# Kernel optimization log

Measured on AMD Instinct MI355X. Metric: run time of the kernel, lower is better.

The kernel has to match this reference:

```python
import jax, jax.numpy as jnp
import numpy as np

N, E = 30000, 480000
HID, NB, D = 256, 128, 2
SW = D * D * NB        # struct-encoder width = bundle_dim^2 * num_bundles = 512
NL, NSAGE = 2, 5       # outer BDL layers, SAGE layers inside struct encoder
OUT = 5
EPS = 1e-5


def _gelu(x):
    return jax.nn.gelu(x, approximate=False)  # torch nn.GELU default (exact)


def _mean_agg(x, src, dst):
    # mean over incoming edges: agg[v] = mean_{u->v} x[u]
    s = jax.ops.segment_sum(x[src], dst, num_segments=N)
    deg = jax.ops.segment_sum(jnp.ones((E,), x.dtype), dst, num_segments=N)
    return s / jnp.maximum(deg, 1.0)[:, None]


def _layernorm(x, g, b):
    m = jnp.mean(x, -1, keepdims=True)
    v = jnp.mean((x - m) ** 2, -1, keepdims=True)
    return (x - m) * jax.lax.rsqrt(v + EPS) * g + b


def _householder(X):
    # torch.nn.utils.parametrizations Orthogonal, orthogonal_map='householder':
    # Q = H_0 H_1 ... H_{d-1}, H_i = I - tau_i v_i v_i^T, v_i = strict-lower col i with unit diag
    d = X.shape[-1]
    A = jnp.tril(X, k=-1)
    tau = 2.0 / (1.0 + jnp.sum(A * A, axis=-2))  # [M, d]
    eye = jnp.eye(d, dtype=X.dtype)
    Q = jnp.broadcast_to(eye, X.shape)
    for i in range(d):
        v = A[:, :, i] + eye[i]
        Qv = jnp.einsum('mij,mj->mi', Q, v)
        Q = Q - tau[:, i, None, None] * Qv[:, :, None] * v[:, None, :]
    return Q


def _struct_encoder(h, src, dst, se_in_w, se_in_b, sage_w1, sage_b1, sage_w2, sage_b2, se_out_w, se_out_b):
    # Model('SAGE', 5, ...) with normalization='None'; dropout inactive in eval
    z = _gelu(h @ se_in_w + se_in_b)
    for i in range(NSAGE):
        m = _mean_agg(z, src, dst)
        zc = jnp.concatenate([z, m], axis=-1)  # SAGE: cat(self, mean(neigh))
        z = z + (_gelu(zc @ sage_w1[i] + sage_b1[i]) @ sage_w2[i] + sage_b2[i])
    return z @ se_out_w + se_out_b


def _forward(x, w_in, b_in, se_in_w, se_in_b, sage_w1, sage_b1, sage_w2, sage_b2,
             se_out_w, se_out_b, enc_w1, enc_b1, enc_w2, enc_b2, ln_g, ln_b,
             bdl_w1, bdl_b1, bdl_w2, bdl_b2, out_ln_g, out_ln_b, w_out, b_out, edge_index):
    src, dst = edge_index[0], edge_index[1]
    h = _gelu(x @ w_in + b_in)
    for k in range(NL):
        enc = _struct_encoder(h, src, dst, se_in_w, se_in_b, sage_w1, sage_b1,
                              sage_w2, sage_b2, se_out_w, se_out_b)
        nr = _gelu(enc @ enc_w1[k] + enc_b1[k]) @ enc_w2[k] + enc_b2[k]  # [N, SW]
        O = _householder(nr.reshape(N * NB, D, D)).reshape(N, NB, D, D)
        # BDL residual module: transport features through per-node bundle frames
        hn = _layernorm(h, ln_g[k], ln_b[k])
        hb = hn.reshape(N, NB, D)
        y = jnp.einsum('nbij,nbj->nbi', O, hb)                       # rotate into frame
        agg = _mean_agg(y.reshape(N, NB * D), src, dst).reshape(N, NB, D)
        msg = jnp.einsum('nbji,nbj->nbi', O, agg).reshape(N, NB * D)  # O^T transports back
        hc = jnp.concatenate([hn, msg], axis=-1)
        h = h + (_gelu(hc @ bdl_w1[k] + bdl_b1[k]) @ bdl_w2[k] + bdl_b2[k])
    h = _layernorm(h, out_ln_g, out_ln_b)
    return h @ w_out + b_out  # [N, OUT]; .squeeze(1) is a no-op for OUT>1


def _w(key, fan_in, shape):
    return jax.random.normal(key, shape, dtype=jnp.float32) / np.sqrt(fan_in)


def setup_inputs() -> dict:
    key = jax.random.key(0)
    ks = iter(jax.random.split(key, 40))
    f32 = jnp.float32
    return {
        'x': jax.random.normal(next(ks), (N, HID), dtype=f32),
        'edge_index': jax.random.randint(next(ks), (2, E), 0, N, dtype=jnp.int32),
        'w_in': _w(next(ks), HID, (HID, HID)), 'b_in': jnp.zeros((HID,), f32),
        'se_in_w': _w(next(ks), HID, (HID, SW)), 'se_in_b': jnp.zeros((SW,), f32),
        'sage_w1': _w(next(ks), 2 * SW, (NSAGE, 2 * SW, SW)), 'sage_b1': jnp.zeros((NSAGE, SW), f32),
        'sage_w2': _w(next(ks), SW, (NSAGE, SW, SW)), 'sage_b2': jnp.zeros((NSAGE, SW), f32),
        'se_out_w': _w(next(ks), SW, (SW, SW)), 'se_out_b': jnp.zeros((SW,), f32),
        'enc_w1': _w(next(ks), SW, (NL, SW, SW)), 'enc_b1': jnp.zeros((NL, SW), f32),
        'enc_w2': _w(next(ks), SW, (NL, SW, SW)), 'enc_b2': jnp.zeros((NL, SW), f32),
        'ln_g': jnp.ones((NL, HID), f32), 'ln_b': jnp.zeros((NL, HID), f32),
        'bdl_w1': _w(next(ks), 2 * HID, (NL, 2 * HID, HID)), 'bdl_b1': jnp.zeros((NL, HID), f32),
        'bdl_w2': _w(next(ks), HID, (NL, HID, HID)), 'bdl_b2': jnp.zeros((NL, HID), f32),
        'out_ln_g': jnp.ones((HID,), f32), 'out_ln_b': jnp.zeros((HID,), f32),
        'w_out': _w(next(ks), HID, (HID, OUT)), 'b_out': jnp.zeros((OUT,), f32),
    }


def reference(x, edge_index, w_in, b_in, se_in_w, se_in_b, sage_w1, sage_b1, sage_w2, sage_b2,
              se_out_w, se_out_b, enc_w1, enc_b1, enc_w2, enc_b2, ln_g, ln_b,
              bdl_w1, bdl_b1, bdl_w2, bdl_b2, out_ln_g, out_ln_b, w_out, b_out):
    return _forward(x, w_in, b_in, se_in_w, se_in_b, sage_w1, sage_b1, sage_w2, sage_b2,
                    se_out_w, se_out_b, enc_w1, enc_b1, enc_w2, enc_b2, ln_g, ln_b,
                    bdl_w1, bdl_b1, bdl_w2, bdl_b2, out_ln_g, out_ln_b, w_out, b_out, edge_index)
```

## Files before the change

kernel.cpp:

```cpp
#include <hip/hip_runtime.h>
#include <hip/hip_bf16.h>
#include <cstdint>
#include <cstddef>


typedef __attribute__((ext_vector_type(8))) short short8;
typedef __attribute__((ext_vector_type(4))) float f32x4;

__device__ __forceinline__ float gelu_exact(float x) {
  return 0.5f * x * (1.0f + erff(x * 0.7071067811865475f));
}
__device__ __forceinline__ unsigned short f2bf(float f) {
  __hip_bfloat16 b = __float2bfloat16(f);
  return *reinterpret_cast<unsigned short*>(&b);
}
__device__ __forceinline__ float bf2f(unsigned short u) {
  return __uint_as_float((unsigned)u << 16);
}
__device__ __forceinline__ float bflo(unsigned u) { return __uint_as_float(u << 16); }
__device__ __forceinline__ float bfhi(unsigned u) { return __uint_as_float(u & 0xffff0000u); }
__device__ __forceinline__ unsigned packbf(float f0, float f1) {
  return (unsigned)f2bf(f0) | ((unsigned)f2bf(f1) << 16);
}
__device__ __forceinline__ void gload16(const void* g, void* l) {
  __builtin_amdgcn_global_load_lds((const __attribute__((address_space(1))) void*)g,
                                   (__attribute__((address_space(3))) void*)l, 16, 0, 0);
}

__global__ void k_hist(const int* __restrict__ dst, int* __restrict__ deg, int E) {
  int i = blockIdx.x * 256 + threadIdx.x;
  if (i < E) atomicAdd(&deg[dst[i]], 1);
}

__global__ __launch_bounds__(1024)
void k_scan(const int* __restrict__ deg, int* __restrict__ rp, int* __restrict__ cur, int Nn) {
  __shared__ int part[1024];
  int t = threadIdx.x;
  int chunk = (Nn + 1023) >> 10;
  int s0 = t * chunk;
  int e0 = s0 + chunk; if (e0 > Nn) e0 = Nn;
  int s = 0;
  for (int i = s0; i < e0; ++i) s += deg[i];
  part[t] = s;
  __syncthreads();
  for (int off = 1; off < 1024; off <<= 1) {
    int v = (t >= off) ? part[t - off] : 0;
    __syncthreads();
    part[t] += v;
    __syncthreads();
  }
  int base = (t == 0) ? 0 : part[t - 1];
  for (int i = s0; i < e0; ++i) {
    rp[i] = base; cur[i] = base; base += deg[i];
  }
  if (t == 0) rp[Nn] = part[1023];
}

__global__ void k_fill(const int* __restrict__ src, const int* __restrict__ dst,
                       int* __restrict__ cur, int* __restrict__ srcs, int E) {
  int i = blockIdx.x * 256 + threadIdx.x;
  if (i < E) {
    int p = atomicAdd(&cur[dst[i]], 1);
    srcs[p] = src[i];
  }
}

__global__ void k_wT(const float* __restrict__ W, unsigned short* __restrict__ Wt, int K, int Nc) {
  int idx = blockIdx.x * 256 + threadIdx.x;
  if (idx >= K * Nc) return;
  int k = idx % K, n = idx / K;
  Wt[(size_t)n * K + k] = f2bf(W[(size_t)k * Nc + n]);
}

__global__ void k_cast(const float* __restrict__ src, unsigned short* __restrict__ dst, int n) {
  int i = blockIdx.x * 256 + threadIdx.x;
  if (i < n) dst[i] = f2bf(src[i]);
}

template<int ACT, bool RES, bool DUAL, bool W32, bool WBF>
__global__ __launch_bounds__(256)
void k_mfma(const unsigned short* __restrict__ A1, const unsigned short* __restrict__ A2,
            int K1, int K2,
            const unsigned short* __restrict__ Wt, const float* __restrict__ bias,
            const float* R, float* C32, unsigned short* Cbf, int M, int Nc) {
  __shared__ unsigned short As[128 * 64];
  __shared__ unsigned short Bs[128 * 64];
  const int tid = threadIdx.x;
  const int lane = tid & 63, wv = tid >> 6;
  const int m0 = blockIdx.x * 128, n0 = blockIdx.y * 128;
  const int wr = (wv >> 1) * 64, wc = (wv & 1) * 64;
  const int rA = lane & 15, kg = lane >> 4;
  const int Ktot = K1 + K2;

  f32x4 acc[4][4];
#pragma unroll
  for (int m = 0; m < 4; ++m)
#pragma unroll
    for (int n = 0; n < 4; ++n)
#pragma unroll
      for (int r = 0; r < 4; ++r) acc[m][n][r] = 0.f;

  for (int k0 = 0; k0 < Ktot; k0 += 64) {
    const unsigned short* Asrc; int kc, lda;
    if (!DUAL || k0 < K1) { Asrc = A1; kc = k0; lda = K1; }
    else                  { Asrc = A2; kc = k0 - K1; lda = K2; }
    __syncthreads();
#pragma unroll
    for (int is = 0; is < 4; ++is) {
      int chunk = is * 256 + tid;
      int row = chunk >> 3, seg = chunk & 7;
      int ks = seg ^ (row & 7);
      int gm = m0 + row; gm = gm < M ? gm : M - 1;
      gload16(Asrc + (size_t)gm * lda + kc + ks * 8,
              (char*)As + (size_t)(is * 256 + (wv << 6)) * 16);
      gload16(Wt + (size_t)(n0 + row) * Ktot + k0 + ks * 8,
              (char*)Bs + (size_t)(is * 256 + (wv << 6)) * 16);
    }
    __syncthreads();
#pragma unroll
    for (int kk = 0; kk < 2; ++kk) {
      short8 af[4], bfr[4];
#pragma unroll
      for (int m = 0; m < 4; ++m) {
        int row = wr + m * 16 + rA;
        int ks = (kk * 4 + kg) ^ (row & 7);
        af[m] = *reinterpret_cast<const short8*>((const char*)As + row * 128 + ks * 16);
      }
#pragma unroll
      for (int n = 0; n < 4; ++n) {
        int col = wc + n * 16 + rA;
        int ks = (kk * 4 + kg) ^ (col & 7);
        bfr[n] = *reinterpret_cast<const short8*>((const char*)Bs + col * 128 + ks * 16);
      }
#pragma unroll
      for (int m = 0; m < 4; ++m)
#pragma unroll
        for (int n = 0; n < 4; ++n)
          acc[m][n] = __builtin_amdgcn_mfma_f32_16x16x32_bf16(af[m], bfr[n], acc[m][n], 0, 0, 0);
    }
  }

#pragma unroll
  for (int m = 0; m < 4; ++m) {
    int gr0 = m0 + wr + m * 16 + kg * 4;
#pragma unroll
    for (int n = 0; n < 4; ++n) {
      int gc = n0 + wc + n * 16 + rA;
      float bv = bias[gc];
#pragma unroll
      for (int r = 0; r < 4; ++r) {
        int gr = gr0 + r;
        if (gr < M) {
          float v = acc[m][n][r] + bv;
          if (ACT == 1) v = gelu_exact(v);
          if (RES) v += R[(size_t)gr * Nc + gc];
          if (W32) C32[(size_t)gr * Nc + gc] = v;
          if (WBF) Cbf[(size_t)gr * Nc + gc] = f2bf(v);
        }
      }
    }
  }
}

template<int W, bool ROT>
__global__ __launch_bounds__(256)
void k_agg(const unsigned short* __restrict__ X, const int* __restrict__ rp,
           const int* __restrict__ srcs, const float* __restrict__ o,
           unsigned short* __restrict__ out, int Nn) {
  int wid = (blockIdx.x * 256 + threadIdx.x) >> 6;
  int lane = threadIdx.x & 63;
  if (wid >= Nn) return;
  constexpr int PE = W / 64;
  float a[PE];
#pragma unroll
  for (int p = 0; p < PE; ++p) a[p] = 0.f;
  int beg = rp[wid], end = rp[wid + 1];
  for (int e = beg; e < end; ++e) {
    int s = srcs[e];
    const unsigned* row = reinterpret_cast<const unsigned*>(X + (size_t)s * W) + lane * (PE / 2);
    if (PE == 8) {
      uint4 v = *reinterpret_cast<const uint4*>(row);
      a[0] += bflo(v.x); a[1] += bfhi(v.x); a[2] += bflo(v.y); a[3] += bfhi(v.y);
      a[4] += bflo(v.z); a[5] += bfhi(v.z); a[6] += bflo(v.w); a[7] += bfhi(v.w);
    } else {
      uint2 v = *reinterpret_cast<const uint2*>(row);
      a[0] += bflo(v.x); a[1] += bfhi(v.x); a[2] += bflo(v.y); a[3] += bfhi(v.y);
    }
  }
  float inv = (end > beg) ? 1.0f / (float)(end - beg) : 0.0f;
#pragma unroll
  for (int p = 0; p < PE; ++p) a[p] *= inv;
  if (ROT) {
    float4 oc = *reinterpret_cast<const float4*>(o + (size_t)wid * 256 + lane * 4);
    float m0 = oc.x * a[0] - oc.y * a[1];
    float m1 = oc.y * a[0] + oc.x * a[1];
    float m2 = oc.z * a[2] - oc.w * a[3];
    float m3 = oc.w * a[2] + oc.z * a[3];
    a[0] = m0; a[1] = m1; a[2] = m2; a[3] = m3;
  }
  unsigned short* op = out + (size_t)wid * W + lane * PE;
  if (PE == 8) {
    uint4 rv;
    rv.x = packbf(a[0], a[1]); rv.y = packbf(a[2], a[3]);
    rv.z = packbf(a[4], a[5]); rv.w = packbf(a[6], a[7]);
    *reinterpret_cast<uint4*>(op) = rv;
  } else {
    uint2 rv;
    rv.x = packbf(a[0], a[1]); rv.y = packbf(a[2], a[3]);
    *reinterpret_cast<uint2*>(op) = rv;
  }
}

__global__ void k_oparams(const unsigned short* __restrict__ nr, float* __restrict__ o, int total) {
  int idx = blockIdx.x * 256 + threadIdx.x;
  if (idx >= total) return;
  float x = bf2f(nr[(size_t)idx * 4 + 2]);
  float inv = 1.0f / (1.0f + x * x);
  o[(size_t)idx * 2]     = (x * x - 1.0f) * inv;
  o[(size_t)idx * 2 + 1] = 2.0f * x * inv;
}

__global__ __launch_bounds__(256)
void k_ln_rot(const float* __restrict__ h, const float* __restrict__ o,
              const float* __restrict__ g, const float* __restrict__ b,
              unsigned short* __restrict__ hn, unsigned short* __restrict__ y, int Nn) {
  int wid = (blockIdx.x * 256 + threadIdx.x) >> 6;
  int lane = threadIdx.x & 63;
  if (wid >= Nn) return;
  float4 v = reinterpret_cast<const float4*>(h + (size_t)wid * 256)[lane];
  float s = v.x + v.y + v.z + v.w;
  float ss = v.x * v.x + v.y * v.y + v.z * v.z + v.w * v.w;
#pragma unroll
  for (int off = 1; off < 64; off <<= 1) { s += __shfl_xor(s, off); ss += __shfl_xor(ss, off); }
  float mean = s * (1.0f / 256.0f);
  float var = ss * (1.0f / 256.0f) - mean * mean;
  float rs = rsqrtf(var + 1e-5f);
  float4 gg = reinterpret_cast<const float4*>(g)[lane];
  float4 bb = reinterpret_cast<const float4*>(b)[lane];
  float h0 = (v.x - mean) * rs * gg.x + bb.x;
  float h1 = (v.y - mean) * rs * gg.y + bb.y;
  float h2 = (v.z - mean) * rs * gg.z + bb.z;
  float h3 = (v.w - mean) * rs * gg.w + bb.w;
  uint2 hv; hv.x = packbf(h0, h1); hv.y = packbf(h2, h3);
  *reinterpret_cast<uint2*>(hn + (size_t)wid * 256 + lane * 4) = hv;
  float4 oc = *reinterpret_cast<const float4*>(o + (size_t)wid * 256 + lane * 4);
  float y0 =  oc.x * h0 + oc.y * h1;
  float y1 = -oc.y * h0 + oc.x * h1;
  float y2 =  oc.z * h2 + oc.w * h3;
  float y3 = -oc.w * h2 + oc.z * h3;
  uint2 yv; yv.x = packbf(y0, y1); yv.y = packbf(y2, y3);
  *reinterpret_cast<uint2*>(y + (size_t)wid * 256 + lane * 4) = yv;
}

__global__ __launch_bounds__(256)
void k_final(const float* __restrict__ h, const float* __restrict__ g,
             const float* __restrict__ b, const float* __restrict__ wout,
             const float* __restrict__ bout, float* __restrict__ out, int Nn) {
  int wid = (blockIdx.x * 256 + threadIdx.x) >> 6;
  int lane = threadIdx.x & 63;
  if (wid >= Nn) return;
  float4 v = reinterpret_cast<const float4*>(h + (size_t)wid * 256)[lane];
  float s = v.x + v.y + v.z + v.w;
  float ss = v.x * v.x + v.y * v.y + v.z * v.z + v.w * v.w;
#pragma unroll
  for (int off = 1; off < 64; off <<= 1) { s += __shfl_xor(s, off); ss += __shfl_xor(ss, off); }
  float mean = s * (1.0f / 256.0f);
  float var = ss * (1.0f / 256.0f) - mean * mean;
  float rs = rsqrtf(var + 1e-5f);
  float4 gg = reinterpret_cast<const float4*>(g)[lane];
  float4 bb = reinterpret_cast<const float4*>(b)[lane];
  float hv[4];
  hv[0] = (v.x - mean) * rs * gg.x + bb.x;
  hv[1] = (v.y - mean) * rs * gg.y + bb.y;
  hv[2] = (v.z - mean) * rs * gg.z + bb.z;
  hv[3] = (v.w - mean) * rs * gg.w + bb.w;
  int c0 = lane * 4;
  float dots[5];
#pragma unroll
  for (int j = 0; j < 5; ++j) {
    float p = hv[0] * wout[(size_t)(c0 + 0) * 5 + j] + hv[1] * wout[(size_t)(c0 + 1) * 5 + j]
            + hv[2] * wout[(size_t)(c0 + 2) * 5 + j] + hv[3] * wout[(size_t)(c0 + 3) * 5 + j];
#pragma unroll
    for (int off = 1; off < 64; off <<= 1) p += __shfl_xor(p, off);
    dots[j] = p;
  }
  if (lane == 0) {
#pragma unroll
    for (int j = 0; j < 5; ++j) out[(size_t)wid * 5 + j] = dots[j] + bout[j];
  }
}

extern "C" void kernel_launch(void* const* d_in, const int* in_sizes, int n_in,
                              void* d_out, int out_size, void* d_ws, size_t ws_size,
                              hipStream_t stream) {
  const float* x       = (const float*)d_in[0];
  const int*   ei      = (const int*)  d_in[1];
  const float* w_in    = (const float*)d_in[2];
  const float* b_in    = (const float*)d_in[3];
  const float* se_in_w = (const float*)d_in[4];
  const float* se_in_b = (const float*)d_in[5];
  const float* sage_w1 = (const float*)d_in[6];
  const float* sage_b1 = (const float*)d_in[7];
  const float* sage_w2 = (const float*)d_in[8];
  const float* sage_b2 = (const float*)d_in[9];
  const float* se_out_w= (const float*)d_in[10];
  const float* se_out_b= (const float*)d_in[11];
  const float* enc_w1  = (const float*)d_in[12];
  const float* enc_b1  = (const float*)d_in[13];
  const float* enc_w2  = (const float*)d_in[14];
  const float* enc_b2  = (const float*)d_in[15];
  const float* ln_g    = (const float*)d_in[16];
  const float* ln_b    = (const float*)d_in[17];
  const float* bdl_w1  = (const float*)d_in[18];
  const float* bdl_b1  = (const float*)d_in[19];
  const float* bdl_w2  = (const float*)d_in[20];
  const float* bdl_b2  = (const float*)d_in[21];
  const float* oln_g   = (const float*)d_in[22];
  const float* oln_b   = (const float*)d_in[23];
  const float* w_out   = (const float*)d_in[24];
  const float* b_out   = (const float*)d_in[25];
  float* out = (float*)d_out;

  const int HID = 256, SW = 512;
  const int N = in_sizes[0] / HID;
  const int E = in_sizes[1] / 2;

  float* ws = (float*)d_ws;
  float* h32 = ws;
  float* z32 = h32 + (size_t)N * HID;
  float* o   = z32 + (size_t)N * SW;
  unsigned short* h_bf = (unsigned short*)(o + (size_t)N * HID);
  unsigned short* z_bf = h_bf + (size_t)N * HID;
  unsigned short* t_bf = z_bf + (size_t)N * SW;
  unsigned short* u_bf = t_bf + (size_t)N * SW;
  unsigned short* wts = u_bf + (size_t)N * SW;
  size_t off = 0;
  unsigned short* wt_in    = wts + off; off += 256 * 256;
  unsigned short* wt_se_in = wts + off; off += 512 * 256;
  unsigned short* wt_sage1 = wts + off; off += (size_t)5 * 512 * 1024;
  unsigned short* wt_sage2 = wts + off; off += (size_t)5 * 512 * 512;
  unsigned short* wt_se_out= wts + off; off += 512 * 512;
  unsigned short* wt_enc1  = wts + off; off += (size_t)2 * 512 * 512;
  unsigned short* wt_enc2  = wts + off; off += (size_t)2 * 512 * 512;
  unsigned short* wt_bdl1  = wts + off; off += (size_t)2 * 256 * 512;
  unsigned short* wt_bdl2  = wts + off; off += (size_t)2 * 256 * 256;
  int* deg  = (int*)(wts + off);
  int* rp   = deg + N;
  int* cur  = rp + N + 1;
  int* srcs = cur + N;
  size_t need = (size_t)((char*)(srcs + E) - (char*)d_ws);
  if (ws_size < need) return;

  unsigned short* xbf = u_bf;
  unsigned short* hn  = z_bf;
  unsigned short* y   = z_bf + (size_t)N * HID;
  unsigned short* msg = t_bf;
  unsigned short* g2  = u_bf;

  const int* esrc = ei;
  const int* edst = ei + E;

  auto cdiv = [](int a, int b) { return (a + b - 1) / b; };
  dim3 blk(256);
  int gm_blocks = cdiv(N, 128);
  dim3 g_g256(gm_blocks, 2);
  dim3 g_g512(gm_blocks, 4);
  int gw = cdiv(N * 64, 256);

  hipMemsetAsync(deg, 0, sizeof(int) * N, stream);
  k_hist<<<cdiv(E, 256), blk, 0, stream>>>(edst, deg, E);
  k_scan<<<1, 1024, 0, stream>>>(deg, rp, cur, N);
  k_fill<<<cdiv(E, 256), blk, 0, stream>>>(esrc, edst, cur, srcs, E);

  auto wT = [&](const float* W, unsigned short* Wt, int K, int Nc) {
    k_wT<<<cdiv(K * Nc, 256), blk, 0, stream>>>(W, Wt, K, Nc);
  };
  wT(w_in, wt_in, 256, 256);
  wT(se_in_w, wt_se_in, 256, 512);
  for (int i = 0; i < 5; ++i) {
    wT(sage_w1 + (size_t)i * 1024 * 512, wt_sage1 + (size_t)i * 512 * 1024, 1024, 512);
    wT(sage_w2 + (size_t)i * 512 * 512,  wt_sage2 + (size_t)i * 512 * 512,  512, 512);
  }
  wT(se_out_w, wt_se_out, 512, 512);
  for (int k = 0; k < 2; ++k) {
    wT(enc_w1 + (size_t)k * 512 * 512, wt_enc1 + (size_t)k * 512 * 512, 512, 512);
    wT(enc_w2 + (size_t)k * 512 * 512, wt_enc2 + (size_t)k * 512 * 512, 512, 512);
    wT(bdl_w1 + (size_t)k * 512 * 256, wt_bdl1 + (size_t)k * 256 * 512, 512, 256);
    wT(bdl_w2 + (size_t)k * 256 * 256, wt_bdl2 + (size_t)k * 256 * 256, 256, 256);
  }
  k_cast<<<cdiv(N * HID, 256), blk, 0, stream>>>(x, xbf, N * HID);

  k_mfma<1, false, false, true, true><<<g_g256, blk, 0, stream>>>(
      xbf, nullptr, 256, 0, wt_in, b_in, nullptr, h32, h_bf, N, 256);

  for (int k = 0; k < 2; ++k) {
    k_mfma<1, false, false, true, true><<<g_g512, blk, 0, stream>>>(
        h_bf, nullptr, 256, 0, wt_se_in, se_in_b, nullptr, z32, z_bf, N, 512);
    for (int i = 0; i < 5; ++i) {
      k_agg<512, false><<<gw, blk, 0, stream>>>(z_bf, rp, srcs, nullptr, t_bf, N);
      k_mfma<1, false, true, false, true><<<g_g512, blk, 0, stream>>>(
          z_bf, t_bf, 512, 512, wt_sage1 + (size_t)i * 512 * 1024,
          sage_b1 + (size_t)i * SW, nullptr, nullptr, u_bf, N, 512);
      k_mfma<0, true, false, true, true><<<g_g512, blk, 0, stream>>>(
          u_bf, nullptr, 512, 0, wt_sage2 + (size_t)i * 512 * 512,
          sage_b2 + (size_t)i * SW, z32, z32, z_bf, N, 512);
    }
    k_mfma<0, false, false, false, true><<<g_g512, blk, 0, stream>>>(
        z_bf, nullptr, 512, 0, wt_se_out, se_out_b, nullptr, nullptr, t_bf, N, 512);
    k_mfma<1, false, false, false, true><<<g_g512, blk, 0, stream>>>(
        t_bf, nullptr, 512, 0, wt_enc1 + (size_t)k * 512 * 512,
        enc_b1 + (size_t)k * SW, nullptr, nullptr, u_bf, N, 512);
    k_mfma<0, false, false, false, true><<<g_g512, blk, 0, stream>>>(
        u_bf, nullptr, 512, 0, wt_enc2 + (size_t)k * 512 * 512,
        enc_b2 + (size_t)k * SW, nullptr, nullptr, t_bf, N, 512);
    k_oparams<<<cdiv(N * 128, 256), blk, 0, stream>>>(t_bf, o, N * 128);
    k_ln_rot<<<gw, blk, 0, stream>>>(h32, o, ln_g + (size_t)k * HID, ln_b + (size_t)k * HID, hn, y, N);
    k_agg<256, true><<<gw, blk, 0, stream>>>(y, rp, srcs, o, msg, N);
    k_mfma<1, false, true, false, true><<<g_g256, blk, 0, stream>>>(
        hn, msg, 256, 256, wt_bdl1 + (size_t)k * 256 * 512,
        bdl_b1 + (size_t)k * HID, nullptr, nullptr, g2, N, 256);
    k_mfma<0, true, false, true, true><<<g_g256, blk, 0, stream>>>(
        g2, nullptr, 256, 0, wt_bdl2 + (size_t)k * 256 * 256,
        bdl_b2 + (size_t)k * HID, h32, h32, h_bf, N, 256);
  }

  k_final<<<gw, blk, 0, stream>>>(h32, oln_g, oln_b, w_out, b_out, out, N);
}
```

Baseline: 2.974 ms.

## Enlarge GEMM tiles to 256x256 with 512 threads and double-buffered LDS

The bf16 MFMA GEMM kernel moves from 128x128 tiles with 4 waves to 256x256 tiles with 8 waves, each wave computing a 128x64 sub-tile. The LDS buffers are doubled so the next K-slice is staged while the current one is consumed, and MFMA bursts are wrapped in s_setprio. The aim is more operand reuse per global load and hiding load latency behind compute. The cost is about 128KB of LDS, one block per CU, and far fewer blocks: about 118 for the 256-wide GEMMs, which can leave many CUs idle.

```diff
diff --git a/kernel.cpp b/kernel.cpp
--- a/kernel.cpp
+++ b/kernel.cpp
@@ -78,80 +78,94 @@
 }
 
 template<int ACT, bool RES, bool DUAL, bool W32, bool WBF>
-__global__ __launch_bounds__(256)
+__global__ __launch_bounds__(512, 1)
 void k_mfma(const unsigned short* __restrict__ A1, const unsigned short* __restrict__ A2,
             int K1, int K2,
             const unsigned short* __restrict__ Wt, const float* __restrict__ bias,
             const float* R, float* C32, unsigned short* Cbf, int M, int Nc) {
-  __shared__ unsigned short As[128 * 64];
-  __shared__ unsigned short Bs[128 * 64];
+  __shared__ unsigned short As[2][256 * 64];
+  __shared__ unsigned short Bs[2][256 * 64];
   const int tid = threadIdx.x;
   const int lane = tid & 63, wv = tid >> 6;
-  const int m0 = blockIdx.x * 128, n0 = blockIdx.y * 128;
-  const int wr = (wv >> 1) * 64, wc = (wv & 1) * 64;
+  const int wm = wv >> 2, wn = wv & 3;
+  const int m0 = blockIdx.x * 256, n0 = blockIdx.y * 256;
   const int rA = lane & 15, kg = lane >> 4;
   const int Ktot = K1 + K2;
-
-  f32x4 acc[4][4];
-#pragma unroll
-  for (int m = 0; m < 4; ++m)
+  const int nt = Ktot >> 6;
+
+  f32x4 acc[8][4];
+#pragma unroll
+  for (int fm = 0; fm < 8; ++fm)
 #pragma unroll
     for (int n = 0; n < 4; ++n)
 #pragma unroll
-      for (int r = 0; r < 4; ++r) acc[m][n][r] = 0.f;
-
-  for (int k0 = 0; k0 < Ktot; k0 += 64) {
+      for (int r = 0; r < 4; ++r) acc[fm][n][r] = 0.f;
+
+  auto stage = [&](int t, int b) {
+    int k0 = t << 6;
     const unsigned short* Asrc; int kc, lda;
     if (!DUAL || k0 < K1) { Asrc = A1; kc = k0; lda = K1; }
     else                  { Asrc = A2; kc = k0 - K1; lda = K2; }
-    __syncthreads();
 #pragma unroll
     for (int is = 0; is < 4; ++is) {
-      int chunk = is * 256 + tid;
+      int chunk = is * 512 + tid;
       int row = chunk >> 3, seg = chunk & 7;
       int ks = seg ^ (row & 7);
       int gm = m0 + row; gm = gm < M ? gm : M - 1;
-      gload16(Asrc + (size_t)gm * lda + kc + ks * 8,
-              (char*)As + (size_t)(is * 256 + (wv << 6)) * 16);
-      gload16(Wt + (size_t)(n0 + row) * Ktot + k0 + ks * 8,
-              (char*)Bs + (size_t)(is * 256 + (wv << 6)) * 16);
+      gload16(Asrc + (size_t)gm * lda + kc + ks * 8, (char*)As[b] + (size_t)chunk * 16);
+      gload16(Wt + (size_t)(n0 + row) * Ktot + k0 + ks * 8, (char*)Bs[b] + (size_t)chunk * 16);
+    }
+  };
+
+  stage(0, 0);
+  __syncthreads();
+
+  for (int t = 0; t < nt; ++t) {
+    const int b = t & 1;
+    if (t + 1 < nt) stage(t + 1, b ^ 1);
+#pragma unroll
+    for (int kk = 0; kk < 2; ++kk) {
+      short8 bfr[4];
+#pragma unroll
+      for (int n = 0; n < 4; ++n) {
+        int col = wn * 64 + n * 16 + rA;
+        int ks = (kk * 4 + kg) ^ (col & 7);
+        bfr[n] = *reinterpret_cast<const short8*>((const char*)Bs[b] + col * 128 + ks * 16);
+      }
+#pragma unroll
+      for (int mq = 0; mq < 2; ++mq) {
+        short8 af[4];
+#pragma unroll
+        for (int m = 0; m < 4; ++m) {
+          int row = wm * 128 + mq * 64 + m * 16 + rA;
+          int ks = (kk * 4 + kg) ^ (row & 7);
+          af[m] = *reinterpret_cast<const short8*>((const char*)As[b] + row * 128 + ks * 16);
+        }
+        __builtin_amdgcn_s_setprio(1);
+#pragma unroll
+        for (int m = 0; m < 4; ++m)
+#pragma unroll
+          for (int n = 0; n < 4; ++n)
+            acc[mq * 4 + m][n] =
+                __builtin_amdgcn_mfma_f32_16x16x32_bf16(af[m], bfr[n], acc[mq * 4 + m][n], 0, 0, 0);
+        __builtin_amdgcn_s_setprio(0);
+      }
     }
     __syncthreads();
-#pragma unroll
-    for (int kk = 0; kk < 2; ++kk) {
-      short8 af[4], bfr[4];
-#pragma unroll
-      for (int m = 0; m < 4; ++m) {
-        int row = wr + m * 16 + rA;
-        int ks = (kk * 4 + kg) ^ (row & 7);
-        af[m] = *reinterpret_cast<const short8*>((const char*)As + row * 128 + ks * 16);
-      }
-#pragma unroll
-      for (int n = 0; n < 4; ++n) {
-        int col = wc + n * 16 + rA;
-        int ks = (kk * 4 + kg) ^ (col & 7);
-        bfr[n] = *reinterpret_cast<const short8*>((const char*)Bs + col * 128 + ks * 16);
-      }
-#pragma unroll
-      for (int m = 0; m < 4; ++m)
-#pragma unroll
-        for (int n = 0; n < 4; ++n)
-          acc[m][n] = __builtin_amdgcn_mfma_f32_16x16x32_bf16(af[m], bfr[n], acc[m][n], 0, 0, 0);
-    }
-  }
-
-#pragma unroll
-  for (int m = 0; m < 4; ++m) {
-    int gr0 = m0 + wr + m * 16 + kg * 4;
+  }
+
+#pragma unroll
+  for (int fm = 0; fm < 8; ++fm) {
+    int gr0 = m0 + wm * 128 + fm * 16 + kg * 4;
 #pragma unroll
     for (int n = 0; n < 4; ++n) {
-      int gc = n0 + wc + n * 16 + rA;
+      int gc = n0 + wn * 64 + n * 16 + rA;
       float bv = bias[gc];
 #pragma unroll
       for (int r = 0; r < 4; ++r) {
         int gr = gr0 + r;
         if (gr < M) {
-          float v = acc[m][n][r] + bv;
+          float v = acc[fm][n][r] + bv;
           if (ACT == 1) v = gelu_exact(v);
           if (RES) v += R[(size_t)gr * Nc + gc];
           if (W32) C32[(size_t)gr * Nc + gc] = v;
@@ -362,9 +376,10 @@
 
   auto cdiv = [](int a, int b) { return (a + b - 1) / b; };
   dim3 blk(256);
-  int gm_blocks = cdiv(N, 128);
-  dim3 g_g256(gm_blocks, 2);
-  dim3 g_g512(gm_blocks, 4);
+  dim3 blk512(512);
+  int gm_blocks = cdiv(N, 256);
+  dim3 g_g256(gm_blocks, 1);
+  dim3 g_g512(gm_blocks, 2);
   int gw = cdiv(N * 64, 256);
 
   hipMemsetAsync(deg, 0, sizeof(int) * N, stream);
@@ -390,36 +405,36 @@
   }
   k_cast<<<cdiv(N * HID, 256), blk, 0, stream>>>(x, xbf, N * HID);
 
-  k_mfma<1, false, false, true, true><<<g_g256, blk, 0, stream>>>(
+  k_mfma<1, false, false, true, true><<<g_g256, blk512, 0, stream>>>(
       xbf, nullptr, 256, 0, wt_in, b_in, nullptr, h32, h_bf, N, 256);
 
   for (int k = 0; k < 2; ++k) {
-    k_mfma<1, false, false, true, true><<<g_g512, blk, 0, stream>>>(
+    k_mfma<1, false, false, true, true><<<g_g512, blk512, 0, stream>>>(
         h_bf, nullptr, 256, 0, wt_se_in, se_in_b, nullptr, z32, z_bf, N, 512);
     for (int i = 0; i < 5; ++i) {
       k_agg<512, false><<<gw, blk, 0, stream>>>(z_bf, rp, srcs, nullptr, t_bf, N);
-      k_mfma<1, false, true, false, true><<<g_g512, blk, 0, stream>>>(
+      k_mfma<1, false, true, false, true><<<g_g512, blk512, 0, stream>>>(
           z_bf, t_bf, 512, 512, wt_sage1 + (size_t)i * 512 * 1024,
           sage_b1 + (size_t)i * SW, nullptr, nullptr, u_bf, N, 512);
-      k_mfma<0, true, false, true, true><<<g_g512, blk, 0, stream>>>(
+      k_mfma<0, true, false, true, true><<<g_g512, blk512, 0, stream>>>(
           u_bf, nullptr, 512, 0, wt_sage2 + (size_t)i * 512 * 512,
           sage_b2 + (size_t)i * SW, z32, z32, z_bf, N, 512);
     }
-    k_mfma<0, false, false, false, true><<<g_g512, blk, 0, stream>>>(
+    k_mfma<0, false, false, false, true><<<g_g512, blk512, 0, stream>>>(
         z_bf, nullptr, 512, 0, wt_se_out, se_out_b, nullptr, nullptr, t_bf, N, 512);
-    k_mfma<1, false, false, false, true><<<g_g512, blk, 0, stream>>>(
+    k_mfma<1, false, false, false, true><<<g_g512, blk512, 0, stream>>>(
         t_bf, nullptr, 512, 0, wt_enc1 + (size_t)k * 512 * 512,
         enc_b1 + (size_t)k * SW, nullptr, nullptr, u_bf, N, 512);
-    k_mfma<0, false, false, false, true><<<g_g512, blk, 0, stream>>>(
+    k_mfma<0, false, false, false, true><<<g_g512, blk512, 0, stream>>>(
         u_bf, nullptr, 512, 0, wt_enc2 + (size_t)k * 512 * 512,
         enc_b2 + (size_t)k * SW, nullptr, nullptr, t_bf, N, 512);
     k_oparams<<<cdiv(N * 128, 256), blk, 0, stream>>>(t_bf, o, N * 128);
     k_ln_rot<<<gw, blk, 0, stream>>>(h32, o, ln_g + (size_t)k * HID, ln_b + (size_t)k * HID, hn, y, N);
     k_agg<256, true><<<gw, blk, 0, stream>>>(y, rp, srcs, o, msg, N);
-    k_mfma<1, false, true, false, true><<<g_g256, blk, 0, stream>>>(
+    k_mfma<1, false, true, false, true><<<g_g256, blk512, 0, stream>>>(
         hn, msg, 256, 256, wt_bdl1 + (size_t)k * 256 * 512,
         bdl_b1 + (size_t)k * HID, nullptr, nullptr, g2, N, 256);
-    k_mfma<0, true, false, true, true><<<g_g256, blk, 0, stream>>>(
+    k_mfma<0, true, false, true, true><<<g_g256, blk512, 0, stream>>>(
         g2, nullptr, 256, 0, wt_bdl2 + (size_t)k * 256 * 256,
         bdl_b2 + (size_t)k * HID, h32, h32, h_bf, N, 256);
   }
```

Result: faster. 2.849 ms (-4.2%).
